# Kernel optimization log

Measured on AMD Instinct MI355X. Metric: run time of the kernel, lower is better.

## Reference

```python
import jax, jax.numpy as jnp
import numpy as np

EPS = 1e-6


def _layernorm(x, g, b):
    mu = jnp.mean(x, axis=-1, keepdims=True)
    var = jnp.mean((x - mu) ** 2, axis=-1, keepdims=True)
    return (x - mu) * jax.lax.rsqrt(var + EPS) * g + b


def _sinusoidal_pe(seq_len, d_model):
    pos = jnp.arange(seq_len, dtype=jnp.float32)[:, None]
    div = jnp.exp(jnp.arange(0, d_model, 2, dtype=jnp.float32) * (-np.log(10000.0) / d_model))
    pe = jnp.zeros((seq_len, d_model), dtype=jnp.float32)
    pe = pe.at[:, 0::2].set(jnp.sin(pos * div))
    pe = pe.at[:, 1::2].set(jnp.cos(pos * div))
    return pe


def setup_inputs() -> dict:
    key = jax.random.key(0)
    ks = jax.random.split(key, 6)
    B, S, D, H = 4, 4096, 1024, 16
    std = 0.02
    return {
        "x": jax.random.normal(ks[0], (B, S, D), jnp.float32),
        "ln1_g": jnp.ones((D,), jnp.float32),
        "ln1_b": jnp.zeros((D,), jnp.float32),
        "w_qkv": jax.random.normal(ks[1], (D, 3 * D), jnp.float32) * std,
        "w_out": jax.random.normal(ks[2], (D, D), jnp.float32) * std,
        "b_out": jnp.zeros((D,), jnp.float32),
        "ln2_g": jnp.ones((D,), jnp.float32),
        "ln2_b": jnp.zeros((D,), jnp.float32),
        "w1": jax.random.normal(ks[3], (D, 2 * D), jnp.float32) * std,
        "b1": jnp.zeros((2 * D,), jnp.float32),
        "w2": jax.random.normal(ks[4], (2 * D, 2 * D), jnp.float32) * std,
        "b2": jnp.zeros((2 * D,), jnp.float32),
        "w3": jax.random.normal(ks[5], (2 * D, D), jnp.float32) * std,
        "b3": jnp.zeros((D,), jnp.float32),
    }


def reference(x, ln1_g, ln1_b, w_qkv, w_out, b_out, ln2_g, ln2_b, w1, b1, w2, b2, w3, b3):
    B, S, D = x.shape
    H = 16
    dh = D // H  # dim_head = 64

    h = _layernorm(x, ln1_g, ln1_b)
    h = h + _sinusoidal_pe(S, D)[None]  # space_dim == 1 -> sinusoidal PE

    # linear (kernelized, non-causal) self-attention: efficient-attention style
    qkv = h @ w_qkv  # [B,S,3D]
    q, k, v = jnp.split(qkv, 3, axis=-1)
    to_heads = lambda t: t.reshape(B, S, H, dh).transpose(0, 2, 1, 3)  # [B,H,S,dh]
    q, k, v = to_heads(q), to_heads(k), to_heads(v)
    q = jax.nn.softmax(q, axis=-1) * (dh ** -0.5)
    k = jax.nn.softmax(k, axis=2)  # softmax over sequence
    context = jnp.einsum('bhnd,bhne->bhde', k, v)  # [B,H,dh,dh]
    attn = jnp.einsum('bhnd,bhde->bhne', q, context)  # [B,H,S,dh]
    attn = attn.transpose(0, 2, 1, 3).reshape(B, S, D)
    attn = attn @ w_out + b_out

    x = x + attn  # residual (dropout p=0)

    y = _layernorm(x, ln2_g, ln2_b)
    y = jax.nn.gelu(y @ w1 + b1, approximate=False)
    y = jax.nn.gelu(y @ w2 + b2, approximate=False)
    y = y @ w3 + b3
    return x + y
```

## Files before the change

### kernel.cpp

```cpp
#include <hip/hip_runtime.h>
#include <cstdint>
#include <cstddef>

#define BB 4
#define SS 4096
#define DD 1024
#define HH 16
#define MM (BB*SS)

typedef __bf16 bf16x8 __attribute__((ext_vector_type(8)));
typedef float  f32x4  __attribute__((ext_vector_type(4)));

__device__ __forceinline__ float b2f(unsigned short h){
    union { unsigned int u; float f; } c; c.u = ((unsigned int)h) << 16; return c.f;
}
__device__ __forceinline__ float b2f_u(unsigned int u16){
    union { unsigned int u; float f; } c; c.u = u16 << 16; return c.f;
}
__device__ __forceinline__ unsigned short f2b(float f){
    union { float f; unsigned int u; } c; c.f = f;
    unsigned int u = c.u + 0x7FFFu + ((c.u >> 16) & 1u);
    return (unsigned short)(u >> 16);
}

__global__ void transpose_cvt(const float* __restrict__ src, unsigned short* __restrict__ dst,
                              int K, int N){
    __shared__ float tile[32][33];
    int kb = blockIdx.y*32, nb = blockIdx.x*32;
    int tx = threadIdx.x, ty = threadIdx.y;
    for(int i=0;i<32;i+=8) tile[ty+i][tx] = src[(size_t)(kb+ty+i)*N + nb+tx];
    __syncthreads();
    for(int i=0;i<32;i+=8) dst[(size_t)(nb+ty+i)*K + kb+tx] = f2b(tile[tx][ty+i]);
}

template<int INBF>
__global__ __launch_bounds__(256) void ln_kernel(const void* __restrict__ xin,
                                                 const float* __restrict__ g,
                                                 const float* __restrict__ bta,
                                                 unsigned short* __restrict__ out,
                                                 int add_pe){
    int row = blockIdx.x;
    int t = threadIdx.x;
    float4 v;
    if (INBF == 0) {
        v = ((const float4*)((const float*)xin + (size_t)row*DD))[t];
    } else {
        ushort4 u = ((const ushort4*)((const unsigned short*)xin + (size_t)row*DD))[t];
        v.x = b2f(u.x); v.y = b2f(u.y); v.z = b2f(u.z); v.w = b2f(u.w);
    }
    float s = v.x+v.y+v.z+v.w;
    float q = v.x*v.x+v.y*v.y+v.z*v.z+v.w*v.w;
    for(int off=32; off>0; off>>=1){ s += __shfl_xor(s, off); q += __shfl_xor(q, off); }
    __shared__ float red[8];
    int wv = t>>6, ln = t&63;
    if(ln==0){ red[wv] = s; red[4+wv] = q; }
    __syncthreads();
    s = red[0]+red[1]+red[2]+red[3];
    q = red[4]+red[5]+red[6]+red[7];
    float mu = s * (1.0f/1024.0f);
    float var = q * (1.0f/1024.0f) - mu*mu;
    float rs = rsqrtf(var + 1e-6f);
    int d0 = t*4;
    float4 gg = ((const float4*)g)[t];
    float4 bb = ((const float4*)bta)[t];
    float o0 = (v.x-mu)*rs*gg.x + bb.x;
    float o1 = (v.y-mu)*rs*gg.y + bb.y;
    float o2 = (v.z-mu)*rs*gg.z + bb.z;
    float o3 = (v.w-mu)*rs*gg.w + bb.w;
    if(add_pe){
        int sidx = row & (SS-1);
        const float cfac = -0.008994473019508968f;
        float a0 = (float)sidx * expf(cfac * (float)(d0));
        float a1 = (float)sidx * expf(cfac * (float)(d0 + 2));
        o0 += sinf(a0); o1 += cosf(a0);
        o2 += sinf(a1); o3 += cosf(a1);
    }
    ushort4 o;
    o.x = f2b(o0); o.y = f2b(o1); o.z = f2b(o2); o.w = f2b(o3);
    *(ushort4*)(out + (size_t)row*DD + d0) = o;
}


#define BARX __builtin_amdgcn_s_barrier()
#define LGK0 { asm volatile("s_waitcnt lgkmcnt(0)" ::: "memory"); __builtin_amdgcn_sched_barrier(0); }
#define LGK8 asm volatile("s_waitcnt lgkmcnt(8)" ::: "memory")
#define VM6  asm volatile("s_waitcnt vmcnt(6)" ::: "memory")
#define PRIO1 __builtin_amdgcn_s_setprio(1)
#define PRIO0 __builtin_amdgcn_s_setprio(0)

#define LDA(D, QR) { \
    const char* _pa = sA + (((D)*2+(QR))<<14) + rbaseA; \
    _Pragma("unroll") \
    for (int mi = 0; mi < 4; mi++) { \
        ra[mi][0] = *(const bf16x8*)(_pa + (mi<<11) + kb0); \
        ra[mi][1] = *(const bf16x8*)(_pa + (mi<<11) + kb1); \
    } }

#define LDB(RB, D, QC) { \
    const char* _pb = sB + (((D)*2+(QC))<<14) + rbaseB; \
    _Pragma("unroll") \
    for (int nj = 0; nj < 2; nj++) { \
        RB[nj][0] = *(const bf16x8*)(_pb + (nj<<11) + kb0); \
        RB[nj][1] = *(const bf16x8*)(_pb + (nj<<11) + kb1); \
    } }

#define MMAC(RB, QR, QC) { \
    _Pragma("unroll") \
    for (int mi = 0; mi < 4; mi++) \
    _Pragma("unroll") \
    for (int nj = 0; nj < 2; nj++) \
    _Pragma("unroll") \
    for (int kk = 0; kk < 2; kk++) \
        acc[(QR)*4+mi][(QC)*2+nj] = __builtin_amdgcn_mfma_f32_16x16x32_bf16( \
            ra[mi][kk], RB[nj][kk], acc[(QR)*4+mi][(QC)*2+nj], 0, 0, 0); }

#define STAGEA(D, H, KS) { \
    __builtin_amdgcn_global_load_lds((const __attribute__((address_space(1))) void*)(pA[H][0] + (KS)), \
        (__attribute__((address_space(3))) void*)(sA + (((D)*2+(H))<<14) + wbase), 16, 0, 0); \
    __builtin_amdgcn_global_load_lds((const __attribute__((address_space(1))) void*)(pA[H][1] + (KS)), \
        (__attribute__((address_space(3))) void*)(sA + (((D)*2+(H))<<14) + wbase + 8192), 16, 0, 0); }

#define STAGEB(D, Q, KS) { \
    __builtin_amdgcn_global_load_lds((const __attribute__((address_space(1))) void*)(pB[Q][0] + (KS)), \
        (__attribute__((address_space(3))) void*)(sB + (((D)*2+(Q))<<14) + wbase), 16, 0, 0); \
    __builtin_amdgcn_global_load_lds((const __attribute__((address_space(1))) void*)(pB[Q][1] + (KS)), \
        (__attribute__((address_space(3))) void*)(sB + (((D)*2+(Q))<<14) + wbase + 8192), 16, 0, 0); }

template<int EPI>
__global__ __launch_bounds__(512, 2) void gemm256(
        const unsigned short* __restrict__ A,
        const unsigned short* __restrict__ Bt,
        void* __restrict__ Cout,
        const float* __restrict__ bias,
        const void* __restrict__ resid,
        int M, int N, int K)
{
    __shared__ __align__(16) unsigned short lAbuf[2*2*128*64];
    __shared__ __align__(16) unsigned short lBbuf[2*2*128*64];
    char* sA = (char*)lAbuf;
    char* sB = (char*)lBbuf;

    const int tid  = threadIdx.x;
    const int lane = tid & 63;
    const int wave = tid >> 6;
    const int quad = lane >> 4;
    const int l16  = lane & 15;
    const int wr = wave >> 2;
    const int wc = wave & 3;

    int gn  = gridDim.x;
    int lin = blockIdx.y * gn + blockIdx.x;
    int xcd = lin & 7;
    int j   = lin >> 3;
    int mt  = xcd + 8*(j/gn);
    int nt  = j - (j/gn)*gn;
    const int m0 = mt * 256;
    const int n0 = nt * 256;

    const unsigned short* pA[2][2];
    const unsigned short* pB[2][2];
    #pragma unroll
    for (int h = 0; h < 2; h++) {
        #pragma unroll
        for (int jj = 0; jj < 2; jj++) {
            int c  = tid + 512*jj;
            int lr = c >> 3;
            int kc = ((c & 7) ^ (lr & 7)) << 3;
            int ga = m0 + ((lr>>6)<<7) + h*64 + (lr & 63);
            int gb = n0 + ((lr>>5)<<6) + h*32 + (lr & 31);
            pA[h][jj] = A  + (size_t)ga * K + kc;
            pB[h][jj] = Bt + (size_t)gb * K + kc;
        }
    }
    const int wbase  = wave << 10;
    const int rbaseA = (wr*64 + l16) * 128;
    const int rbaseB = (wc*32 + l16) * 128;
    const int kb0 = (quad*16)      ^ ((l16 & 7) << 4);
    const int kb1 = (64 + quad*16) ^ ((l16 & 7) << 4);

    f32x4 acc[8][4] = {};
    bf16x8 ra[4][2], rb0[2][2], rb1[2][2];

    STAGEA(0,0, 0); STAGEB(0,0, 0); STAGEB(0,1, 0); STAGEA(0,1, 0);
    STAGEA(1,0, 64); STAGEB(1,0, 64); STAGEB(1,1, 64);
    VM6;
    BARX;

    const int NIT = K >> 7;
    for (int it = 0; it < NIT; it++) {
        int ka  = it << 7;
        int kb_ = ka + 64;
        int kc2 = ka + 128; if (kc2 >= K) kc2 = 0;
        int kc3 = ka + 192; if (kc3 >= K) kc3 = 0;

        LDA(0,0); LDB(rb0, 0,0);
        STAGEA(1,1, kb_);
        LGK8;
        BARX; LGK0; PRIO1; MMAC(rb0, 0,0); PRIO0; BARX;
        LDB(rb1, 0,1);
        STAGEA(0,0, kc2);
        BARX; LGK0; PRIO1; MMAC(rb1, 0,1); PRIO0; BARX;
        LDA(0,1);
        STAGEB(0,0, kc2);
        BARX; LGK0; PRIO1; MMAC(rb1, 1,1); PRIO0; BARX;
        STAGEB(0,1, kc2);
        VM6;
        BARX; LGK0; PRIO1; MMAC(rb0, 1,0); PRIO0; BARX;
        LDA(1,0); LDB(rb0, 1,0);
        STAGEA(0,1, kc2);
        LGK8;
        BARX; LGK0; PRIO1; MMAC(rb0, 0,0); PRIO0; BARX;
        LDB(rb1, 1,1);
        STAGEA(1,0, kc3);
        BARX; LGK0; PRIO1; MMAC(rb1, 0,1); PRIO0; BARX;
        LDA(1,1);
        STAGEB(1,0, kc3);
        BARX; LGK0; PRIO1; MMAC(rb1, 1,1); PRIO0; BARX;
        STAGEB(1,1, kc3);
        VM6;
        BARX; LGK0; PRIO1; MMAC(rb0, 1,0); PRIO0; BARX;
    }
    asm volatile("s_waitcnt vmcnt(0)" ::: "memory");

    #pragma unroll
    for (int qm = 0; qm < 8; qm++) {
        int grow0 = m0 + wr*128 + (qm>>2)*64 + (qm&3)*16 + quad*4;
        #pragma unroll
        for (int r = 0; r < 4; r++) {
            int grow = grow0 + r;
            #pragma unroll
            for (int ni = 0; ni < 4; ni++) {
                int gcol = n0 + wc*64 + ni*16 + l16;
                float v = acc[qm][ni][r];
                size_t idx = (size_t)grow * N + gcol;
                if (EPI == 0) {
                    ((unsigned short*)Cout)[idx] = f2b(v);
                } else if (EPI == 1) {
                    v += bias[gcol];
                    v = 0.5f * v * (1.0f + erff(v * 0.70710678118654752f));
                    ((unsigned short*)Cout)[idx] = f2b(v);
                } else if (EPI == 2) {
                    v += bias[gcol] + ((const float*)resid)[idx];
                    ((unsigned short*)Cout)[idx] = f2b(v);
                } else {
                    v += bias[gcol] + b2f(((const unsigned short*)resid)[idx]);
                    ((float*)Cout)[idx] = v;
                }
            }
        }
    }
}

__global__ __launch_bounds__(256) void ctx_partial(const unsigned short* __restrict__ qkv,
                                                   float* __restrict__ EP,
                                                   float* __restrict__ CS){
    int sc = blockIdx.x, h = blockIdx.y, b = blockIdx.z;
    int t = threadIdx.x;
    __shared__ __align__(16) float kl[64][64];
    __shared__ __align__(16) float vl[64][64];
    __shared__ float csred[4][64];
    float acc[4][4] = {};
    float cspart = 0.0f;
    int e4 = (t & 15) * 4, d4 = (t >> 4) * 4;
    int dcol = t & 63, schunk = t >> 6;
    for(int s0 = 0; s0 < 256; s0 += 64){
        __syncthreads();
        #pragma unroll
        for(int j=0;j<2;j++){
            int lin = t + 256*j;
            int row = lin >> 3;
            int c8  = (lin & 7) * 8;
            size_t gr = (size_t)(b*SS + sc*256 + s0 + row);
            uint4 kv = *(const uint4*)(qkv + gr*3072 + DD + h*64 + c8);
            float4 ka, kb2;
            ka.x = expf(b2f_u(kv.x & 0xFFFFu)); ka.y = expf(b2f_u(kv.x >> 16));
            ka.z = expf(b2f_u(kv.y & 0xFFFFu)); ka.w = expf(b2f_u(kv.y >> 16));
            kb2.x = expf(b2f_u(kv.z & 0xFFFFu)); kb2.y = expf(b2f_u(kv.z >> 16));
            kb2.z = expf(b2f_u(kv.w & 0xFFFFu)); kb2.w = expf(b2f_u(kv.w >> 16));
            *(float4*)&kl[row][c8]   = ka;
            *(float4*)&kl[row][c8+4] = kb2;
            uint4 vv = *(const uint4*)(qkv + gr*3072 + 2*DD + h*64 + c8);
            float4 va, vb;
            va.x = b2f_u(vv.x & 0xFFFFu); va.y = b2f_u(vv.x >> 16);
            va.z = b2f_u(vv.y & 0xFFFFu); va.w = b2f_u(vv.y >> 16);
            vb.x = b2f_u(vv.z & 0xFFFFu); vb.y = b2f_u(vv.z >> 16);
            vb.z = b2f_u(vv.w & 0xFFFFu); vb.w = b2f_u(vv.w >> 16);
            *(float4*)&vl[row][c8]   = va;
            *(float4*)&vl[row][c8+4] = vb;
        }
        __syncthreads();
        #pragma unroll
        for(int i=0;i<16;i++) cspart += kl[schunk*16+i][dcol];
        for(int s=0;s<64;s++){
            float4 k4 = *(const float4*)&kl[s][d4];
            float4 v4 = *(const float4*)&vl[s][e4];
            acc[0][0] += k4.x*v4.x; acc[0][1] += k4.x*v4.y; acc[0][2] += k4.x*v4.z; acc[0][3] += k4.x*v4.w;
            acc[1][0] += k4.y*v4.x; acc[1][1] += k4.y*v4.y; acc[1][2] += k4.y*v4.z; acc[1][3] += k4.y*v4.w;
            acc[2][0] += k4.z*v4.x; acc[2][1] += k4.z*v4.y; acc[2][2] += k4.z*v4.z; acc[2][3] += k4.z*v4.w;
            acc[3][0] += k4.w*v4.x; acc[3][1] += k4.w*v4.y; acc[3][2] += k4.w*v4.z; acc[3][3] += k4.w*v4.w;
        }
    }
    int slot = (b*HH + h)*16 + sc;
    float* ep = EP + (size_t)slot*4096;
    #pragma unroll
    for(int i=0;i<4;i++)
        *(float4*)&ep[(d4+i)*64 + e4] = *(float4*)&acc[i][0];
    csred[schunk][dcol] = cspart;
    __syncthreads();
    if(t < 64) CS[slot*64 + t] = csred[0][t]+csred[1][t]+csred[2][t]+csred[3][t];
}

__global__ __launch_bounds__(256) void ctx_reduce(const float* __restrict__ EP,
                                                  const float* __restrict__ CS,
                                                  float* __restrict__ CTXF){
    int bh = blockIdx.x;
    int t = threadIdx.x;
    int d = t >> 2, e0 = (t & 3) * 16;
    float cs = 0.0f;
    #pragma unroll
    for(int sl=0; sl<16; sl++) cs += CS[(bh*16+sl)*64 + d];
    float inv = 1.0f/cs;
    #pragma unroll
    for(int i=0;i<16;i++){
        float s = 0.0f;
        #pragma unroll
        for(int sl=0; sl<16; sl++) s += EP[(size_t)(bh*16+sl)*4096 + d*64 + e0 + i];
        CTXF[(size_t)bh*4096 + d*64 + e0 + i] = s * inv;
    }
}

__global__ __launch_bounds__(256) void attn_heads(const unsigned short* __restrict__ qkv,
                                                  const float* __restrict__ CTXF,
                                                  unsigned short* __restrict__ abuf){
    int rg = blockIdx.x, h = blockIdx.y;
    int b = rg >> 6;
    int t = threadIdx.x;
    __shared__ __align__(16) float cl[64][64];
    __shared__ __align__(16) float qlT[64*68];
    const float* cb = CTXF + (size_t)(b*HH + h)*4096;
    for(int j=0;j<4;j++){
        int lin = t + 256*j;
        ((float4*)cl)[lin] = ((const float4*)cb)[lin];
    }
    {
        int r = t >> 2, seg = (t & 3) * 16;
        const unsigned short* qp = qkv + (size_t)(rg*64 + r)*3072 + h*64 + seg;
        float vals[16];
        float m = -1e30f;
        #pragma unroll
        for(int u=0; u<4; u++){
            ushort4 qv = *(const ushort4*)(qp + u*4);
            vals[u*4+0]=b2f(qv.x); vals[u*4+1]=b2f(qv.y); vals[u*4+2]=b2f(qv.z); vals[u*4+3]=b2f(qv.w);
        }
        #pragma unroll
        for(int i=0;i<16;i++) m = fmaxf(m, vals[i]);
        m = fmaxf(m, __shfl_xor(m, 1));
        m = fmaxf(m, __shfl_xor(m, 2));
        float ssum = 0.0f;
        #pragma unroll
        for(int i=0;i<16;i++){ vals[i] = expf(vals[i]-m); ssum += vals[i]; }
        ssum += __shfl_xor(ssum, 1);
        ssum += __shfl_xor(ssum, 2);
        float scl = 0.125f/ssum;
        #pragma unroll
        for(int i=0;i<16;i++) qlT[(seg+i)*68 + r] = vals[i]*scl;
    }
    __syncthreads();
    int e4 = (t & 15) * 4, r4 = (t >> 4) * 4;
    float acc[4][4] = {};
    for(int d=0; d<64; d++){
        float4 q4 = *(const float4*)&qlT[d*68 + r4];
        float4 c4 = *(const float4*)&cl[d][e4];
        acc[0][0] += q4.x*c4.x; acc[0][1] += q4.x*c4.y; acc[0][2] += q4.x*c4.z; acc[0][3] += q4.x*c4.w;
        acc[1][0] += q4.y*c4.x; acc[1][1] += q4.y*c4.y; acc[1][2] += q4.y*c4.z; acc[1][3] += q4.y*c4.w;
        acc[2][0] += q4.z*c4.x; acc[2][1] += q4.z*c4.y; acc[2][2] += q4.z*c4.z; acc[2][3] += q4.z*c4.w;
        acc[3][0] += q4.w*c4.x; acc[3][1] += q4.w*c4.y; acc[3][2] += q4.w*c4.z; acc[3][3] += q4.w*c4.w;
    }
    #pragma unroll
    for(int i=0;i<4;i++){
        ushort4 o;
        o.x = f2b(acc[i][0]); o.y = f2b(acc[i][1]); o.z = f2b(acc[i][2]); o.w = f2b(acc[i][3]);
        *(ushort4*)(abuf + (size_t)(rg*64 + r4 + i)*DD + h*64 + e4) = o;
    }
}

extern "C" void kernel_launch(void* const* d_in, const int* in_sizes, int n_in,
                              void* d_out, int out_size, void* d_ws, size_t ws_size,
                              hipStream_t stream)
{
    const float* x     = (const float*)d_in[0];
    const float* ln1_g = (const float*)d_in[1];
    const float* ln1_b = (const float*)d_in[2];
    const float* w_qkv = (const float*)d_in[3];
    const float* w_out = (const float*)d_in[4];
    const float* b_out = (const float*)d_in[5];
    const float* ln2_g = (const float*)d_in[6];
    const float* ln2_b = (const float*)d_in[7];
    const float* w1    = (const float*)d_in[8];
    const float* b1    = (const float*)d_in[9];
    const float* w2    = (const float*)d_in[10];
    const float* b2    = (const float*)d_in[11];
    const float* w3    = (const float*)d_in[12];
    const float* b3    = (const float*)d_in[13];

    char* ws = (char*)d_ws;
    unsigned short* wqkvT = (unsigned short*)(ws + 0);
    unsigned short* woutT = (unsigned short*)(ws + 6291456);
    unsigned short* w1T   = (unsigned short*)(ws + 8388608);
    unsigned short* w2T   = (unsigned short*)(ws + 12582912);
    unsigned short* w3T   = (unsigned short*)(ws + 20971520);
    unsigned short* Hbuf  = (unsigned short*)(ws + 25165824);
    unsigned short* QKV   = (unsigned short*)(ws + 58720256);
    float*          EP    = (float*)(ws + 159383552);
    float*          CS    = (float*)(ws + 176160768);
    float*          CTXF  = (float*)(ws + 176422912);
    unsigned short* Abuf  = Hbuf;
    unsigned short* X2    = (unsigned short*)(ws + 58720256);
    unsigned short* H2    = Hbuf;
    unsigned short* Y1    = (unsigned short*)d_out;
    unsigned short* Y2    = (unsigned short*)(ws + 125829120);

    dim3 tb(32, 8);
    transpose_cvt<<<dim3(3072/32, 1024/32), tb, 0, stream>>>(w_qkv, wqkvT, 1024, 3072);
    transpose_cvt<<<dim3(1024/32, 1024/32), tb, 0, stream>>>(w_out, woutT, 1024, 1024);
    transpose_cvt<<<dim3(2048/32, 1024/32), tb, 0, stream>>>(w1,    w1T,   1024, 2048);
    transpose_cvt<<<dim3(2048/32, 2048/32), tb, 0, stream>>>(w2,    w2T,   2048, 2048);
    transpose_cvt<<<dim3(1024/32, 2048/32), tb, 0, stream>>>(w3,    w3T,   2048, 1024);

    ln_kernel<0><<<MM, 256, 0, stream>>>(x, ln1_g, ln1_b, Hbuf, 1);

    gemm256<0><<<dim3(3072/256, MM/256), 512, 0, stream>>>(Hbuf, wqkvT, QKV, nullptr, nullptr, MM, 3072, 1024);

    ctx_partial<<<dim3(16, HH, BB), 256, 0, stream>>>(QKV, EP, CS);
    ctx_reduce<<<BB*HH, 256, 0, stream>>>(EP, CS, CTXF);
    attn_heads<<<dim3(256, HH), 256, 0, stream>>>(QKV, CTXF, Abuf);

    gemm256<2><<<dim3(1024/256, MM/256), 512, 0, stream>>>(Abuf, woutT, X2, b_out, x, MM, 1024, 1024);

    ln_kernel<1><<<MM, 256, 0, stream>>>(X2, ln2_g, ln2_b, H2, 0);

    gemm256<1><<<dim3(2048/256, MM/256), 512, 0, stream>>>(H2, w1T, Y1, b1, nullptr, MM, 2048, 1024);
    gemm256<1><<<dim3(2048/256, MM/256), 512, 0, stream>>>(Y1, w2T, Y2, b2, nullptr, MM, 2048, 2048);
    gemm256<3><<<dim3(1024/256, MM/256), 512, 0, stream>>>(Y2, w3T, d_out, b3, X2, MM, 1024, 2048);
}
```

Before: 745.8 us.

## Software-pipeline LDS fragment loads ahead of MFMA blocks in GEMM main loop

Restructures the bf16 GEMM inner loop so the LDS-to-register loads for the next quadrant are issued before the current MFMA block runs, using extra register buffers (L0/L1/T/U/V) instead of waiting on lgkmcnt(0) before each MFMA group. It cuts one barrier per phase, reorders global-to-LDS staging, and computes staging addresses from a single base pointer rather than precomputed pointer arrays. The aim is to hide LDS latency and barrier stalls behind matrix math. In exchange it raises register pressure at 2 blocks per CU and depends on correct vmcnt accounting for the reordered stages.

```diff
diff --git a/kernel.cpp b/kernel.cpp
--- a/kernel.cpp
+++ b/kernel.cpp
@@ -82,49 +82,61 @@
 
 
 #define BARX __builtin_amdgcn_s_barrier()
-#define LGK0 { asm volatile("s_waitcnt lgkmcnt(0)" ::: "memory"); __builtin_amdgcn_sched_barrier(0); }
-#define LGK8 asm volatile("s_waitcnt lgkmcnt(8)" ::: "memory")
+#define SCB  __builtin_amdgcn_sched_barrier(0)
 #define VM6  asm volatile("s_waitcnt vmcnt(6)" ::: "memory")
+#define VM4  asm volatile("s_waitcnt vmcnt(4)" ::: "memory")
 #define PRIO1 __builtin_amdgcn_s_setprio(1)
 #define PRIO0 __builtin_amdgcn_s_setprio(0)
 
-#define LDA(D, QR) { \
-    const char* _pa = sA + (((D)*2+(QR))<<14) + rbaseA; \
-    _Pragma("unroll") \
-    for (int mi = 0; mi < 4; mi++) { \
-        ra[mi][0] = *(const bf16x8*)(_pa + (mi<<11) + kb0); \
-        ra[mi][1] = *(const bf16x8*)(_pa + (mi<<11) + kb1); \
-    } }
-
-#define LDB(RB, D, QC) { \
-    const char* _pb = sB + (((D)*2+(QC))<<14) + rbaseB; \
-    _Pragma("unroll") \
-    for (int nj = 0; nj < 2; nj++) { \
-        RB[nj][0] = *(const bf16x8*)(_pb + (nj<<11) + kb0); \
-        RB[nj][1] = *(const bf16x8*)(_pb + (nj<<11) + kb1); \
-    } }
-
-#define MMAC(RB, QR, QC) { \
-    _Pragma("unroll") \
-    for (int mi = 0; mi < 4; mi++) \
+#define STGA(D, H, KS) { \
+    const unsigned short* _s0 = baseA + (size_t)((H)*64)*K + (KS); \
+    const unsigned short* _s1 = baseA + (size_t)((H)*64+128)*K + (KS); \
+    char* _d = ((char*)lA) + (((D)*2+(H))<<14) + wbase; \
+    __builtin_amdgcn_global_load_lds((const __attribute__((address_space(1))) void*)_s0, \
+        (__attribute__((address_space(3))) void*)_d, 16, 0, 0); \
+    __builtin_amdgcn_global_load_lds((const __attribute__((address_space(1))) void*)_s1, \
+        (__attribute__((address_space(3))) void*)(_d + 8192), 16, 0, 0); }
+
+#define STGB(D, Q, KS) { \
+    const unsigned short* _s0 = baseB + (size_t)((Q)*32)*K + (KS); \
+    const unsigned short* _s1 = baseB + (size_t)((Q)*32+128)*K + (KS); \
+    char* _d = ((char*)lB) + (((D)*2+(Q))<<14) + wbase; \
+    __builtin_amdgcn_global_load_lds((const __attribute__((address_space(1))) void*)_s0, \
+        (__attribute__((address_space(3))) void*)_d, 16, 0, 0); \
+    __builtin_amdgcn_global_load_lds((const __attribute__((address_space(1))) void*)_s1, \
+        (__attribute__((address_space(3))) void*)(_d + 8192), 16, 0, 0); }
+
+#define LDAm(DST, D, H, MI0) { \
+    const char* _p = ((const char*)lA) + (((D)*2+(H))<<14) + rbaseA; \
+    DST[0][0] = *(const bf16x8*)(_p + ((MI0)<<11) + kb0); \
+    DST[0][1] = *(const bf16x8*)(_p + ((MI0)<<11) + kb1); \
+    DST[1][0] = *(const bf16x8*)(_p + (((MI0)+1)<<11) + kb0); \
+    DST[1][1] = *(const bf16x8*)(_p + (((MI0)+1)<<11) + kb1); }
+
+#define LDBm(DST, D, Q) { \
+    const char* _p = ((const char*)lB) + (((D)*2+(Q))<<14) + rbaseB; \
+    DST[0][0] = *(const bf16x8*)(_p + kb0); \
+    DST[0][1] = *(const bf16x8*)(_p + kb1); \
+    DST[1][0] = *(const bf16x8*)(_p + 2048 + kb0); \
+    DST[1][1] = *(const bf16x8*)(_p + 2048 + kb1); }
+
+#define MMQ(LS, TS, BS, QH, QB) { \
+    _Pragma("unroll") \
+    for (int mi = 0; mi < 2; mi++) \
     _Pragma("unroll") \
     for (int nj = 0; nj < 2; nj++) \
     _Pragma("unroll") \
     for (int kk = 0; kk < 2; kk++) \
-        acc[(QR)*4+mi][(QC)*2+nj] = __builtin_amdgcn_mfma_f32_16x16x32_bf16( \
-            ra[mi][kk], RB[nj][kk], acc[(QR)*4+mi][(QC)*2+nj], 0, 0, 0); }
-
-#define STAGEA(D, H, KS) { \
-    __builtin_amdgcn_global_load_lds((const __attribute__((address_space(1))) void*)(pA[H][0] + (KS)), \
-        (__attribute__((address_space(3))) void*)(sA + (((D)*2+(H))<<14) + wbase), 16, 0, 0); \
-    __builtin_amdgcn_global_load_lds((const __attribute__((address_space(1))) void*)(pA[H][1] + (KS)), \
-        (__attribute__((address_space(3))) void*)(sA + (((D)*2+(H))<<14) + wbase + 8192), 16, 0, 0); }
-
-#define STAGEB(D, Q, KS) { \
-    __builtin_amdgcn_global_load_lds((const __attribute__((address_space(1))) void*)(pB[Q][0] + (KS)), \
-        (__attribute__((address_space(3))) void*)(sB + (((D)*2+(Q))<<14) + wbase), 16, 0, 0); \
-    __builtin_amdgcn_global_load_lds((const __attribute__((address_space(1))) void*)(pB[Q][1] + (KS)), \
-        (__attribute__((address_space(3))) void*)(sB + (((D)*2+(Q))<<14) + wbase + 8192), 16, 0, 0); }
+        acc[(QH)*4+mi][(QB)*2+nj] = __builtin_amdgcn_mfma_f32_16x16x32_bf16( \
+            LS[mi][kk], BS[nj][kk], acc[(QH)*4+mi][(QB)*2+nj], 0, 0, 0); \
+    _Pragma("unroll") \
+    for (int mi = 0; mi < 2; mi++) \
+    _Pragma("unroll") \
+    for (int nj = 0; nj < 2; nj++) \
+    _Pragma("unroll") \
+    for (int kk = 0; kk < 2; kk++) \
+        acc[(QH)*4+2+mi][(QB)*2+nj] = __builtin_amdgcn_mfma_f32_16x16x32_bf16( \
+            TS[mi][kk], BS[nj][kk], acc[(QH)*4+2+mi][(QB)*2+nj], 0, 0, 0); }
 
 template<int EPI>
 __global__ __launch_bounds__(512, 2) void gemm256(
@@ -135,10 +147,8 @@
         const void* __restrict__ resid,
         int M, int N, int K)
 {
-    __shared__ __align__(16) unsigned short lAbuf[2*2*128*64];
-    __shared__ __align__(16) unsigned short lBbuf[2*2*128*64];
-    char* sA = (char*)lAbuf;
-    char* sB = (char*)lBbuf;
+    __shared__ __align__(16) unsigned short lA[4*128*64];
+    __shared__ __align__(16) unsigned short lB[4*128*64];
 
     const int tid  = threadIdx.x;
     const int lane = tid & 63;
@@ -157,68 +167,67 @@
     const int m0 = mt * 256;
     const int n0 = nt * 256;
 
-    const unsigned short* pA[2][2];
-    const unsigned short* pB[2][2];
-    #pragma unroll
-    for (int h = 0; h < 2; h++) {
-        #pragma unroll
-        for (int jj = 0; jj < 2; jj++) {
-            int c  = tid + 512*jj;
-            int lr = c >> 3;
-            int kc = ((c & 7) ^ (lr & 7)) << 3;
-            int ga = m0 + ((lr>>6)<<7) + h*64 + (lr & 63);
-            int gb = n0 + ((lr>>5)<<6) + h*32 + (lr & 31);
-            pA[h][jj] = A  + (size_t)ga * K + kc;
-            pB[h][jj] = Bt + (size_t)gb * K + kc;
-        }
-    }
-    const int wbase  = wave << 10;
+    const int r8  = tid >> 3;
+    const int kcE = ((tid & 7) ^ (r8 & 7)) << 3;
+    const unsigned short* baseA = A  + ((size_t)(m0 + r8) * K + kcE);
+    const int gb0 = ((r8 >> 5) << 6) + (r8 & 31);
+    const unsigned short* baseB = Bt + ((size_t)(n0 + gb0) * K + kcE);
+    const int wbase = wave << 10;
+
     const int rbaseA = (wr*64 + l16) * 128;
     const int rbaseB = (wc*32 + l16) * 128;
     const int kb0 = (quad*16)      ^ ((l16 & 7) << 4);
     const int kb1 = (64 + quad*16) ^ ((l16 & 7) << 4);
 
     f32x4 acc[8][4] = {};
-    bf16x8 ra[4][2], rb0[2][2], rb1[2][2];
-
-    STAGEA(0,0, 0); STAGEB(0,0, 0); STAGEB(0,1, 0); STAGEA(0,1, 0);
-    STAGEA(1,0, 64); STAGEB(1,0, 64); STAGEB(1,1, 64);
+    bf16x8 L0[2][2], L1[2][2], T[2][2], U[2][2], V[2][2];
+
+    STGA(0,0, 0); STGB(0,1, 0); STGB(0,0, 0); STGA(0,1, 0);
+    STGA(1,0, 64); STGB(1,1, 64);
     VM6;
-    BARX;
+    BARX; SCB;
+    LDAm(L0, 0,0, 0);
+    LDBm(U,  0,0);
 
     const int NIT = K >> 7;
     for (int it = 0; it < NIT; it++) {
         int ka  = it << 7;
-        int kb_ = ka + 64;
+        int kd1 = ka + 64;
         int kc2 = ka + 128; if (kc2 >= K) kc2 = 0;
         int kc3 = ka + 192; if (kc3 >= K) kc3 = 0;
 
-        LDA(0,0); LDB(rb0, 0,0);
-        STAGEA(1,1, kb_);
-        LGK8;
-        BARX; LGK0; PRIO1; MMAC(rb0, 0,0); PRIO0; BARX;
-        LDB(rb1, 0,1);
-        STAGEA(0,0, kc2);
-        BARX; LGK0; PRIO1; MMAC(rb1, 0,1); PRIO0; BARX;
-        LDA(0,1);
-        STAGEB(0,0, kc2);
-        BARX; LGK0; PRIO1; MMAC(rb1, 1,1); PRIO0; BARX;
-        STAGEB(0,1, kc2);
-        VM6;
-        BARX; LGK0; PRIO1; MMAC(rb0, 1,0); PRIO0; BARX;
-        LDA(1,0); LDB(rb0, 1,0);
-        STAGEA(0,1, kc2);
-        LGK8;
-        BARX; LGK0; PRIO1; MMAC(rb0, 0,0); PRIO0; BARX;
-        LDB(rb1, 1,1);
-        STAGEA(1,0, kc3);
-        BARX; LGK0; PRIO1; MMAC(rb1, 0,1); PRIO0; BARX;
-        LDA(1,1);
-        STAGEB(1,0, kc3);
-        BARX; LGK0; PRIO1; MMAC(rb1, 1,1); PRIO0; BARX;
-        STAGEB(1,1, kc3);
-        VM6;
-        BARX; LGK0; PRIO1; MMAC(rb0, 1,0); PRIO0; BARX;
+        STGB(1,0, kd1);
+        LDAm(T, 0,0, 2); LDBm(V, 0,1);
+        PRIO1; MMQ(L0, T, U, 0,0); PRIO0;
+        VM6; BARX; SCB;
+        STGA(1,1, kd1);
+        LDAm(L1, 0,1, 0);
+        PRIO1; MMQ(L0, T, V, 0,1); PRIO0;
+        BARX; SCB;
+        STGA(0,0, kc2);
+        LDAm(T, 0,1, 2); LDBm(U, 0,0);
+        PRIO1; MMQ(L1, T, V, 1,1); PRIO0;
+        VM4; BARX; SCB;
+        STGB(0,1, kc2);
+        LDAm(L0, 1,0, 0); LDBm(V, 1,0);
+        PRIO1; MMQ(L1, T, U, 1,0); PRIO0;
+        BARX; SCB;
+        STGB(0,0, kc2);
+        LDAm(T, 1,0, 2); LDBm(U, 1,1);
+        PRIO1; MMQ(L0, T, V, 0,0); PRIO0;
+        VM6; BARX; SCB;
+        STGA(0,1, kc2);
+        LDAm(L1, 1,1, 0);
+        PRIO1; MMQ(L0, T, U, 0,1); PRIO0;
+        BARX; SCB;
+        STGA(1,0, kc3);
+        LDAm(T, 1,1, 2); LDBm(V, 1,0);
+        PRIO1; MMQ(L1, T, U, 1,1); PRIO0;
+        VM4; BARX; SCB;
+        STGB(1,1, kc3);
+        LDAm(L0, 0,0, 0); LDBm(U, 0,0);
+        PRIO1; MMQ(L1, T, V, 1,0); PRIO0;
+        BARX; SCB;
     }
     asm volatile("s_waitcnt vmcnt(0)" ::: "memory");
 
```

New measurement: 739.9 us. Within noise of the previous version (-0.8%).
